# Kernel optimization log

Hardware: AMD Instinct MI355X
Metric: run time of the kernel (lower is better)

The kernel has to match this reference:

```python
import jax, jax.numpy as jnp
import numpy as np

HIDDEN_DIM = 128

def custom_softmax(x, axis):
    e = jnp.exp(x)
    e = jnp.where(jnp.isinf(e), jnp.float32(1e30), e)
    s = jnp.sum(e, axis=axis, keepdims=True)
    return e / (s + 1e-14)

def setup_inputs() -> dict:
    key = jax.random.key(0)
    k1, k2, k3, kq, kk, kv = jax.random.split(key, 6)
    B, L, D = 4, 4096, 256
    x1 = jax.random.normal(k1, (B, L, D), dtype=jnp.float32)
    x2 = jax.random.normal(k2, (B, L, D), dtype=jnp.float32)
    x3 = jax.random.normal(k3, (B, L, D), dtype=jnp.float32)
    mask = jnp.zeros((L, L), dtype=jnp.float32)
    # nn.Linear(D, H, bias=False): kaiming-uniform-ish init, stored as [D, H] for x @ W
    lim = 1.0 / np.sqrt(D)
    Wq = jax.random.uniform(kq, (D, HIDDEN_DIM), jnp.float32, -lim, lim)
    Wk = jax.random.uniform(kk, (D, HIDDEN_DIM), jnp.float32, -lim, lim)
    Wv = jax.random.uniform(kv, (D, HIDDEN_DIM), jnp.float32, -lim, lim)
    return {"x1": x1, "x2": x2, "x3": x3, "mask": mask, "Wq": Wq, "Wk": Wk, "Wv": Wv}

def reference(x1, x2, x3, mask, Wq, Wk, Wv):
    q = jnp.einsum('bld,dh->blh', x1, Wq)
    k = jnp.einsum('bld,dh->blh', x2, Wk)
    v = jnp.einsum('bld,dh->blh', x3, Wv)
    scale = 1.0 / jnp.sqrt(jnp.float32(HIDDEN_DIM))
    scores = jnp.einsum('bqh,bkh->bqk', q, k) * scale  # [B, L, L]
    weights = custom_softmax(scores + mask, axis=-1)
    return jnp.einsum('bqk,bkh->bqh', weights, v)
```

## Files before the change

kernel.cpp:

```cpp
#include <hip/hip_runtime.h>
#include <hip/hip_bf16.h>

typedef __attribute__((ext_vector_type(8))) short bf16x8;
typedef __attribute__((ext_vector_type(4))) float f32x4;

#define QSCALE 0.088388347648318447f

static __device__ __forceinline__ f32x4 mfma16(bf16x8 a, bf16x8 b, f32x4 c) {
    return __builtin_amdgcn_mfma_f32_16x16x32_bf16(a, b, c, 0, 0, 0);
}

union BF8 { bf16x8 v; __hip_bfloat16 b[8]; };

__global__ void wt_kernel(const float* __restrict__ Wq, const float* __restrict__ Wk,
                          const float* __restrict__ Wv, __hip_bfloat16* __restrict__ wt)
{
    const int w = blockIdx.y;
    const float* W = (w == 0) ? Wq : ((w == 1) ? Wk : Wv);
    const int e = blockIdx.x * 256 + threadIdx.x;
    const int h = e >> 8, d = e & 255;
    wt[w * 32768 + e] = __float2bfloat16(W[d * 128 + h]);
}

__global__ __launch_bounds__(256, 3) void proj_kernel(
    const float* __restrict__ x1, const float* __restrict__ x2, const float* __restrict__ x3,
    const __hip_bfloat16* __restrict__ wt,
    __hip_bfloat16* __restrict__ q_ws, __hip_bfloat16* __restrict__ k_ws,
    __hip_bfloat16* __restrict__ vt_ws)
{
    __shared__ __align__(16) __hip_bfloat16 t_lds[64 * 136];
    const int mode = blockIdx.y;
    const float* x = (mode == 0) ? x1 : ((mode == 1) ? x2 : x3);
    const __hip_bfloat16* wp = wt + mode * 32768;
    const int tid = threadIdx.x, wid = tid >> 6, lane = tid & 63;
    const int l15 = lane & 15, lhi = lane >> 4;
    const int m0 = blockIdx.x * 64 + wid * 16;

    bf16x8 xa[8];
    const float* xr = x + (size_t)(m0 + l15) * 256;
    #pragma unroll
    for (int ks = 0; ks < 8; ks++) {
        const int d0 = ks * 32 + lhi * 8;
        const float4 lo = *(const float4*)(xr + d0);
        const float4 hi = *(const float4*)(xr + d0 + 4);
        BF8 pk;
        pk.b[0] = __float2bfloat16(lo.x); pk.b[1] = __float2bfloat16(lo.y);
        pk.b[2] = __float2bfloat16(lo.z); pk.b[3] = __float2bfloat16(lo.w);
        pk.b[4] = __float2bfloat16(hi.x); pk.b[5] = __float2bfloat16(hi.y);
        pk.b[6] = __float2bfloat16(hi.z); pk.b[7] = __float2bfloat16(hi.w);
        xa[ks] = pk.v;
    }

    f32x4 acc[8];
    #pragma unroll
    for (int hg = 0; hg < 8; hg++) acc[hg] = (f32x4){0.f, 0.f, 0.f, 0.f};

    #pragma unroll
    for (int hg = 0; hg < 8; hg++) {
        #pragma unroll
        for (int ks = 0; ks < 8; ks++) {
            const bf16x8 wb = *(const bf16x8*)(wp + (hg * 16 + l15) * 256 + ks * 32 + lhi * 8);
            acc[hg] = mfma16(xa[ks], wb, acc[hg]);
        }
    }

    if (mode < 2) {
        __hip_bfloat16* outp = (mode == 0) ? q_ws : k_ws;
        const float osc = (mode == 0) ? QSCALE : 1.0f;
        #pragma unroll
        for (int hg = 0; hg < 8; hg++)
            #pragma unroll
            for (int r = 0; r < 4; r++)
                outp[(size_t)(m0 + lhi * 4 + r) * 128 + hg * 16 + l15] =
                    __float2bfloat16(acc[hg][r] * osc);
    } else {
        #pragma unroll
        for (int hg = 0; hg < 8; hg++)
            #pragma unroll
            for (int r = 0; r < 4; r++)
                t_lds[(wid * 16 + lhi * 4 + r) * 136 + hg * 16 + l15] =
                    __float2bfloat16(acc[hg][r]);
        __syncthreads();
        const int b  = (blockIdx.x * 64) >> 12;
        const int l0 = (blockIdx.x * 64) & 4095;
        const int h = tid >> 1, lh = (tid & 1) * 32;
        #pragma unroll
        for (int c = 0; c < 4; c++) {
            BF8 ov;
            #pragma unroll
            for (int j = 0; j < 8; j++) ov.b[j] = t_lds[(lh + c * 8 + j) * 136 + h];
            *(bf16x8*)(vt_ws + (size_t)(b * 128 + h) * 4096 + l0 + lh + c * 8) = ov.v;
        }
    }
}

__global__ __launch_bounds__(256, 1) void attn_kernel(
    const __hip_bfloat16* __restrict__ q_ws,
    const __hip_bfloat16* __restrict__ k_ws,
    const __hip_bfloat16* __restrict__ vt_ws,
    float* __restrict__ dst,
    float* __restrict__ l_ws,
    const int nsplit)
{
    __shared__ __align__(16) __hip_bfloat16 k_lds[64 * 128];
    __shared__ __align__(16) __hip_bfloat16 v_lds[128 * 64];
    __shared__ __align__(16) __hip_bfloat16 p_lds[4][32 * 64];

    const int tid = threadIdx.x, wid = tid >> 6, lane = tid & 63;
    const int l15 = lane & 15, lhi = lane >> 4;
    const int qt = blockIdx.x, b = blockIdx.y, sp = blockIdx.z;
    const int q0 = qt * 128 + wid * 32;

    bf16x8 qa[2][4];
    #pragma unroll
    for (int s = 0; s < 2; s++)
        #pragma unroll
        for (int c = 0; c < 4; c++)
            qa[s][c] = *(const bf16x8*)(q_ws +
                (size_t)(b * 4096 + q0 + s * 16 + l15) * 128 + c * 32 + lhi * 8);

    f32x4 o[2][8];
    #pragma unroll
    for (int s = 0; s < 2; s++)
        #pragma unroll
        for (int hg = 0; hg < 8; hg++) o[s][hg] = (f32x4){0.f, 0.f, 0.f, 0.f};
    float rs[2][4] = {{0.f,0.f,0.f,0.f},{0.f,0.f,0.f,0.f}};

    const int ntile = 64 / nsplit;
    const int kbase = sp * (4096 / nsplit);

    const int kkey = tid >> 4, kcc = tid & 15;
    const int vh = tid >> 3, vcc = tid & 7;
    const __hip_bfloat16* kbp = k_ws + (size_t)b * 4096 * 128;
    const __hip_bfloat16* vbp = vt_ws + (size_t)b * 128 * 4096;

    bf16x8 kpre[4], vpre[4];
    auto issue = [&](int k0) {
        #pragma unroll
        for (int p = 0; p < 4; p++) {
            kpre[p] = *(const bf16x8*)(kbp + (size_t)(k0 + kkey + p * 16) * 128 + kcc * 8);
            vpre[p] = *(const bf16x8*)(vbp + (size_t)(vh + p * 32) * 4096 + k0 + vcc * 8);
        }
    };
    auto commit = [&]() {
        #pragma unroll
        for (int p = 0; p < 4; p++) {
            const int key = kkey + p * 16;
            *(bf16x8*)&k_lds[key * 128 + (((kcc >> 1) ^ (key & 7)) << 4) + ((kcc & 1) << 3)] = kpre[p];
            const int h = vh + p * 32;
            *(bf16x8*)&v_lds[h * 64 + (((vcc >> 1) ^ (h & 3)) << 4) + ((vcc & 1) << 3)] = vpre[p];
        }
    };

    issue(kbase);

    for (int kt = 0; kt < ntile; kt++) {
        __syncthreads();
        commit();
        if (kt + 1 < ntile) issue(kbase + (kt + 1) * 64);
        __syncthreads();

        #pragma unroll
        for (int kg = 0; kg < 4; kg++) {
            f32x4 s0 = (f32x4){0.f,0.f,0.f,0.f};
            f32x4 s1 = (f32x4){0.f,0.f,0.f,0.f};
            const int key = kg * 16 + l15;
            #pragma unroll
            for (int c = 0; c < 4; c++) {
                const int chunk = (c << 1) | (lhi >> 1);
                const bf16x8 kb = *(const bf16x8*)&k_lds[key * 128 +
                    ((chunk ^ (key & 7)) << 4) + ((lhi & 1) << 3)];
                s0 = mfma16(qa[0][c], kb, s0);
                s1 = mfma16(qa[1][c], kb, s1);
            }
            #pragma unroll
            for (int r = 0; r < 4; r++) {
                float e0 = __expf(s0[r]); e0 = fminf(e0, 1e30f);
                float e1 = __expf(s1[r]); e1 = fminf(e1, 1e30f);
                rs[0][r] += e0; rs[1][r] += e1;
                const int row0 = lhi * 4 + r;
                p_lds[wid][row0 * 64 + ((kg ^ lhi) << 4) + l15] = __float2bfloat16(e0);
                p_lds[wid][(row0 + 16) * 64 + ((kg ^ lhi) << 4) + l15] = __float2bfloat16(e1);
            }
        }

        bf16x8 pa[2][2];
        #pragma unroll
        for (int s = 0; s < 2; s++)
            #pragma unroll
            for (int ks = 0; ks < 2; ks++) {
                const int prow = s * 16 + l15;
                const int chunk = (ks << 1) | (lhi >> 1);
                pa[s][ks] = *(const bf16x8*)&p_lds[wid][prow * 64 +
                    ((chunk ^ (l15 >> 2)) << 4) + ((lhi & 1) << 3)];
            }

        #pragma unroll
        for (int hg = 0; hg < 8; hg++) {
            #pragma unroll
            for (int ks = 0; ks < 2; ks++) {
                const int h = hg * 16 + l15;
                const int chunk = (ks << 1) | (lhi >> 1);
                const bf16x8 vb = *(const bf16x8*)&v_lds[h * 64 +
                    ((chunk ^ (h & 3)) << 4) + ((lhi & 1) << 3)];
                o[0][hg] = mfma16(pa[0][ks], vb, o[0][hg]);
                o[1][hg] = mfma16(pa[1][ks], vb, o[1][hg]);
            }
        }
    }

    #pragma unroll
    for (int s = 0; s < 2; s++)
        #pragma unroll
        for (int r = 0; r < 4; r++) {
            float v = rs[s][r];
            v += __shfl_xor(v, 1);
            v += __shfl_xor(v, 2);
            v += __shfl_xor(v, 4);
            v += __shfl_xor(v, 8);
            rs[s][r] = v;
        }

    if (nsplit > 1) {
        const int bq = (sp * 4 + b) * 4096 + q0;
        #pragma unroll
        for (int s = 0; s < 2; s++)
            #pragma unroll
            for (int r = 0; r < 4; r++)
                #pragma unroll
                for (int hg = 0; hg < 8; hg++)
                    dst[(size_t)(bq + s * 16 + lhi * 4 + r) * 128 + hg * 16 + l15] = o[s][hg][r];
        if (l15 == 0) {
            #pragma unroll
            for (int s = 0; s < 2; s++)
                #pragma unroll
                for (int r = 0; r < 4; r++)
                    l_ws[bq + s * 16 + lhi * 4 + r] = rs[s][r];
        }
    } else {
        const int bq = b * 4096 + q0;
        #pragma unroll
        for (int s = 0; s < 2; s++)
            #pragma unroll
            for (int r = 0; r < 4; r++) {
                const float inv = 1.0f / (rs[s][r] + 1e-14f);
                #pragma unroll
                for (int hg = 0; hg < 8; hg++)
                    dst[(size_t)(bq + s * 16 + lhi * 4 + r) * 128 + hg * 16 + l15] =
                        o[s][hg][r] * inv;
            }
    }
}

__global__ void combine_kernel(const float4* __restrict__ num_ws, const float* __restrict__ l_ws,
                               float4* __restrict__ out, const int nsplit)
{
    const int idx = blockIdx.x * 256 + threadIdx.x;
    const int bq = idx >> 5;
    float4 n = {0.f, 0.f, 0.f, 0.f};
    float l = 1e-14f;
    for (int s = 0; s < nsplit; s++) {
        const float4 t = num_ws[idx + s * 524288];
        n.x += t.x; n.y += t.y; n.z += t.z; n.w += t.w;
        l += l_ws[bq + s * 16384];
    }
    const float inv = 1.0f / l;
    out[idx] = (float4){n.x * inv, n.y * inv, n.z * inv, n.w * inv};
}

extern "C" void kernel_launch(void* const* d_in, const int* in_sizes, int n_in,
                              void* d_out, int out_size, void* d_ws, size_t ws_size,
                              hipStream_t stream)
{
    const float* x1 = (const float*)d_in[0];
    const float* x2 = (const float*)d_in[1];
    const float* x3 = (const float*)d_in[2];
    const float* Wq = (const float*)d_in[4];
    const float* Wk = (const float*)d_in[5];
    const float* Wv = (const float*)d_in[6];
    float* out = (float*)d_out;

    char* ws = (char*)d_ws;
    __hip_bfloat16* q_ws  = (__hip_bfloat16*)(ws + 0);
    __hip_bfloat16* k_ws  = (__hip_bfloat16*)(ws + (4u  << 20));
    __hip_bfloat16* vt_ws = (__hip_bfloat16*)(ws + (8u  << 20));
    __hip_bfloat16* wt_ws = (__hip_bfloat16*)(ws + (12u << 20));
    float* num_ws = (float*)(ws + (13u << 20));
    const size_t num_bytes4 = 4ull * (8u << 20);
    const size_t num_bytes2 = 2ull * (8u << 20);

    int nsplit = 1;
    size_t l_off;
    if (ws_size >= (13u << 20) + num_bytes4 + (1u << 20)) { nsplit = 4; l_off = (13u << 20) + num_bytes4; }
    else if (ws_size >= (13u << 20) + num_bytes2 + (1u << 20)) { nsplit = 2; l_off = (13u << 20) + num_bytes2; }
    else { l_off = (13u << 20); }
    float* l_ws = (float*)(ws + l_off);

    wt_kernel<<<dim3(128, 3), 256, 0, stream>>>(Wq, Wk, Wv, wt_ws);
    proj_kernel<<<dim3(256, 3), 256, 0, stream>>>(x1, x2, x3, wt_ws, q_ws, k_ws, vt_ws);
    if (nsplit > 1) {
        attn_kernel<<<dim3(32, 4, nsplit), 256, 0, stream>>>(q_ws, k_ws, vt_ws, num_ws, l_ws, nsplit);
        combine_kernel<<<2048, 256, 0, stream>>>((const float4*)num_ws, l_ws, (float4*)out, nsplit);
    } else {
        attn_kernel<<<dim3(32, 4, 1), 256, 0, stream>>>(q_ws, k_ws, vt_ws, out, l_ws, 1);
    }
}
```

Baseline: 212.3 us.

## Fold scale and log2e into Wq, pipeline projection weights, use raw exp2, setprio

Folds the softmax scale together with log2(e) into the transposed Wq so the attention kernel can call the hardware v_exp_f32 (a base-2 exponent) directly instead of __expf. The projection kernel now processes one output group at a time and double-buffers the weight fragments in registers, which lowers register pressure and overlaps the next loads with the MFMAs. MFMA sections are raised in priority with s_setprio, and the key split count can rise to 8 when the workspace is large enough, adding more parallel blocks at the cost of more partial-result traffic in the combine step. The bf16 rounding of the prescaled weights changes the numerics slightly.

```diff
diff --git a/kernel.cpp b/kernel.cpp
--- a/kernel.cpp
+++ b/kernel.cpp
@@ -5,6 +5,7 @@
 typedef __attribute__((ext_vector_type(4))) float f32x4;
 
 #define QSCALE 0.088388347648318447f
+#define LOG2E  1.4426950408889634f
 
 static __device__ __forceinline__ f32x4 mfma16(bf16x8 a, bf16x8 b, f32x4 c) {
     return __builtin_amdgcn_mfma_f32_16x16x32_bf16(a, b, c, 0, 0, 0);
@@ -17,9 +18,10 @@
 {
     const int w = blockIdx.y;
     const float* W = (w == 0) ? Wq : ((w == 1) ? Wk : Wv);
+    const float sc = (w == 0) ? (QSCALE * LOG2E) : 1.0f;
     const int e = blockIdx.x * 256 + threadIdx.x;
     const int h = e >> 8, d = e & 255;
-    wt[w * 32768 + e] = __float2bfloat16(W[d * 128 + h]);
+    wt[w * 32768 + e] = __float2bfloat16(W[d * 128 + h] * sc);
 }
 
 __global__ __launch_bounds__(256, 3) void proj_kernel(
@@ -51,35 +53,41 @@
         xa[ks] = pk.v;
     }
 
-    f32x4 acc[8];
-    #pragma unroll
-    for (int hg = 0; hg < 8; hg++) acc[hg] = (f32x4){0.f, 0.f, 0.f, 0.f};
-
-    #pragma unroll
+    __hip_bfloat16* outp = (mode == 0) ? q_ws : k_ws;
+
+    bf16x8 wcur[8], wnxt[8];
+    #pragma unroll
+    for (int ks = 0; ks < 8; ks++)
+        wcur[ks] = *(const bf16x8*)(wp + (size_t)l15 * 256 + ks * 32 + lhi * 8);
+
+    #pragma unroll 1
     for (int hg = 0; hg < 8; hg++) {
-        #pragma unroll
-        for (int ks = 0; ks < 8; ks++) {
-            const bf16x8 wb = *(const bf16x8*)(wp + (hg * 16 + l15) * 256 + ks * 32 + lhi * 8);
-            acc[hg] = mfma16(xa[ks], wb, acc[hg]);
-        }
-    }
-
-    if (mode < 2) {
-        __hip_bfloat16* outp = (mode == 0) ? q_ws : k_ws;
-        const float osc = (mode == 0) ? QSCALE : 1.0f;
-        #pragma unroll
-        for (int hg = 0; hg < 8; hg++)
+        if (hg < 7) {
+            #pragma unroll
+            for (int ks = 0; ks < 8; ks++)
+                wnxt[ks] = *(const bf16x8*)(wp + (size_t)((hg + 1) * 16 + l15) * 256 + ks * 32 + lhi * 8);
+        }
+        f32x4 acc = (f32x4){0.f, 0.f, 0.f, 0.f};
+        #pragma unroll
+        for (int ks = 0; ks < 8; ks++)
+            acc = mfma16(xa[ks], wcur[ks], acc);
+
+        if (mode < 2) {
             #pragma unroll
             for (int r = 0; r < 4; r++)
                 outp[(size_t)(m0 + lhi * 4 + r) * 128 + hg * 16 + l15] =
-                    __float2bfloat16(acc[hg][r] * osc);
-    } else {
-        #pragma unroll
-        for (int hg = 0; hg < 8; hg++)
+                    __float2bfloat16(acc[r]);
+        } else {
             #pragma unroll
             for (int r = 0; r < 4; r++)
                 t_lds[(wid * 16 + lhi * 4 + r) * 136 + hg * 16 + l15] =
-                    __float2bfloat16(acc[hg][r]);
+                    __float2bfloat16(acc[r]);
+        }
+        #pragma unroll
+        for (int ks = 0; ks < 8; ks++) wcur[ks] = wnxt[ks];
+    }
+
+    if (mode == 2) {
         __syncthreads();
         const int b  = (blockIdx.x * 64) >> 12;
         const int l0 = (blockIdx.x * 64) & 4095;
@@ -165,6 +173,7 @@
             f32x4 s0 = (f32x4){0.f,0.f,0.f,0.f};
             f32x4 s1 = (f32x4){0.f,0.f,0.f,0.f};
             const int key = kg * 16 + l15;
+            __builtin_amdgcn_s_setprio(1);
             #pragma unroll
             for (int c = 0; c < 4; c++) {
                 const int chunk = (c << 1) | (lhi >> 1);
@@ -173,10 +182,14 @@
                 s0 = mfma16(qa[0][c], kb, s0);
                 s1 = mfma16(qa[1][c], kb, s1);
             }
+            __builtin_amdgcn_s_setprio(0);
             #pragma unroll
             for (int r = 0; r < 4; r++) {
-                float e0 = __expf(s0[r]); e0 = fminf(e0, 1e30f);
-                float e1 = __expf(s1[r]); e1 = fminf(e1, 1e30f);
+                float e0, e1;
+                asm("v_exp_f32 %0, %1" : "=v"(e0) : "v"(s0[r]));
+                asm("v_exp_f32 %0, %1" : "=v"(e1) : "v"(s1[r]));
+                e0 = fminf(e0, 1e30f);
+                e1 = fminf(e1, 1e30f);
                 rs[0][r] += e0; rs[1][r] += e1;
                 const int row0 = lhi * 4 + r;
                 p_lds[wid][row0 * 64 + ((kg ^ lhi) << 4) + l15] = __float2bfloat16(e0);
@@ -195,6 +208,7 @@
                     ((chunk ^ (l15 >> 2)) << 4) + ((lhi & 1) << 3)];
             }
 
+        __builtin_amdgcn_s_setprio(1);
         #pragma unroll
         for (int hg = 0; hg < 8; hg++) {
             #pragma unroll
@@ -207,6 +221,7 @@
                 o[1][hg] = mfma16(pa[1][ks], vb, o[1][hg]);
             }
         }
+        __builtin_amdgcn_s_setprio(0);
     }
 
     #pragma unroll
@@ -286,14 +301,15 @@
     __hip_bfloat16* vt_ws = (__hip_bfloat16*)(ws + (8u  << 20));
     __hip_bfloat16* wt_ws = (__hip_bfloat16*)(ws + (12u << 20));
     float* num_ws = (float*)(ws + (13u << 20));
+    const size_t num_bytes8 = 8ull * (8u << 20);
     const size_t num_bytes4 = 4ull * (8u << 20);
     const size_t num_bytes2 = 2ull * (8u << 20);
 
     int nsplit = 1;
-    size_t l_off;
-    if (ws_size >= (13u << 20) + num_bytes4 + (1u << 20)) { nsplit = 4; l_off = (13u << 20) + num_bytes4; }
+    size_t l_off = (13u << 20);
+    if (ws_size >= (13u << 20) + num_bytes8 + (1u << 20)) { nsplit = 8; l_off = (13u << 20) + num_bytes8; }
+    else if (ws_size >= (13u << 20) + num_bytes4 + (1u << 20)) { nsplit = 4; l_off = (13u << 20) + num_bytes4; }
     else if (ws_size >= (13u << 20) + num_bytes2 + (1u << 20)) { nsplit = 2; l_off = (13u << 20) + num_bytes2; }
-    else { l_off = (13u << 20); }
     float* l_ws = (float*)(ws + l_off);
 
     wt_kernel<<<dim3(128, 3), 256, 0, stream>>>(Wq, Wk, Wv, wt_ws);
```

New measurement: 217.9 us. +2.6%, slower.
